# Kernel tuning notes

Hardware: AMD Instinct MI355X
Metric: run time of the kernel (lower is better)

## Reference

```python
import jax, jax.numpy as jnp
import numpy as np

N_POINTS = 300000
N_PAIRS = 100000  # rulebook pairs per kernel offset
K_OFFSETS = 27    # 3x3x3 kernel
C_IN, C_OUT = 32, 64
GROUPS = 8
EPS = 1e-5
NEG_SLOPE = 0.01


def setup_inputs() -> dict:
    key = jax.random.key(0)
    k1, k2, k3, k4 = jax.random.split(key, 4)
    feats = jax.random.normal(k1, (N_POINTS, C_IN), dtype=jnp.float32)
    weight = jax.random.normal(k2, (K_OFFSETS, C_IN, C_OUT), dtype=jnp.float32) * (1.0 / np.sqrt(C_IN * K_OFFSETS))
    gamma = jnp.ones((C_OUT,), dtype=jnp.float32)
    beta = jnp.zeros((C_OUT,), dtype=jnp.float32)
    in_idx = jax.random.randint(k3, (K_OFFSETS, N_PAIRS), 0, N_POINTS, dtype=jnp.int64)
    out_idx = jax.random.randint(k4, (K_OFFSETS, N_PAIRS), 0, N_POINTS, dtype=jnp.int64)
    return {"feats": feats, "weight": weight, "gamma": gamma, "beta": beta,
            "in_idx": in_idx, "out_idx": out_idx}


def reference(feats, weight, gamma, beta, in_idx, out_idx):
    # Sparse 3D conv via rulebook: gather -> per-offset matmul -> scatter-add
    gathered = feats[in_idx]                       # [K, P, C_in]
    y = jnp.einsum('kpi,kio->kpo', gathered, weight)  # [K, P, C_out]
    out = jnp.zeros((feats.shape[0], weight.shape[2]), feats.dtype)
    out = out.at[out_idx.reshape(-1)].add(y.reshape(-1, weight.shape[2]))
    # GroupNorm(8, C_out): stats over all points and channels within each group
    N, C = out.shape
    xg = out.reshape(N, GROUPS, C // GROUPS)
    mean = jnp.mean(xg, axis=(0, 2), keepdims=True)
    var = jnp.var(xg, axis=(0, 2), keepdims=True)
    xn = ((xg - mean) * jax.lax.rsqrt(var + EPS)).reshape(N, C)
    xn = xn * gamma + beta
    # LeakyReLU (default negative_slope = 0.01)
    return jnp.where(xn >= 0, xn, NEG_SLOPE * xn)
```

## Files before the change

kernel.cpp:

```cpp
#include <hip/hip_runtime.h>

#define NPTS   300000
#define NPAIRS 100000
#define KOFF   27
#define NTOT   (KOFF * NPAIRS)
#define CIN    32
#define COUT   64
#define NGROUP 8
#define EPSV   1e-5f
#define SLOPE  0.01f

#define PAIRS_PER_BLOCK 256
#define BLOCKS_PER_K ((NPAIRS + PAIRS_PER_BLOCK - 1) / PAIRS_PER_BLOCK)
#define NB1 293

#define OFS_STATS  0u
#define OFS_CURSOR 4096u
#define OFS_PART   (OFS_CURSOR + 1204224u)
#define OFS_ENT    (OFS_PART + 4096u)
#define OFS_FH16   (OFS_ENT + 10850304u)
#define WS_MAIN    ((size_t)OFS_FH16 + 19200000u)
#define OFS_FB16_FB 4096u
#define WS_BF16_FB ((size_t)OFS_FB16_FB + 19200000u)

typedef _Float16 half2v __attribute__((ext_vector_type(2)));

__device__ inline unsigned pack_h2(float a, float b) {
    union { _Float16 h[2]; unsigned u; } x;
    x.h[0] = (_Float16)a; x.h[1] = (_Float16)b;
    return x.u;
}
__device__ inline half2v as_h2(unsigned u) {
    union { unsigned u; half2v h; } x; x.u = u; return x.h;
}
__device__ inline float dot2_h(unsigned a, unsigned b, float c) {
#if __has_builtin(__builtin_amdgcn_fdot2)
    return __builtin_amdgcn_fdot2(as_h2(a), as_h2(b), c, false);
#else
    half2v ha = as_h2(a), hb = as_h2(b);
    c = fmaf((float)ha.x, (float)hb.x, c);
    return fmaf((float)ha.y, (float)hb.y, c);
#endif
}
__device__ inline unsigned short f2b(float x) {
    unsigned u = __float_as_uint(x);
    u += 0x7FFFu + ((u >> 16) & 1u);
    return (unsigned short)(u >> 16);
}
__device__ inline float b2f_lo(unsigned d) { return __uint_as_float(d << 16); }
__device__ inline float b2f_hi(unsigned d) { return __uint_as_float(d & 0xFFFF0000u); }


__global__ __launch_bounds__(256) void to_f16_kernel(const float2* __restrict__ src,
                                                     unsigned* __restrict__ dst, int n2) {
    int i = blockIdx.x * 256 + threadIdx.x;
    if (i < n2) { float2 v = src[i]; dst[i] = pack_h2(v.x, v.y); }
}

__global__ __launch_bounds__(256) void zero_aux_kernel(int* __restrict__ cursor,
                                                       float* __restrict__ stats) {
    int i = blockIdx.x * 256 + threadIdx.x;
    if (i < NPTS) cursor[i] = 0;
    if (blockIdx.x == 0 && threadIdx.x < 16) stats[threadIdx.x] = 0.f;
}

__global__ __launch_bounds__(256) void hist_kernel(const int* __restrict__ oi,
                                                   int* __restrict__ cursor) {
    int i = blockIdx.x * 256 + threadIdx.x;
    if (i < NTOT) atomicAdd(cursor + oi[i], 1);
}

__global__ __launch_bounds__(256) void reduce_blocks_kernel(const int* __restrict__ cursor,
                                                            int* __restrict__ part) {
    __shared__ int sm[256];
    int tid = threadIdx.x, i0 = blockIdx.x * 1024 + tid * 4;
    int s = 0;
#pragma unroll
    for (int j = 0; j < 4; ++j) if (i0 + j < NPTS) s += cursor[i0 + j];
    sm[tid] = s; __syncthreads();
    for (int off = 128; off; off >>= 1) {
        if (tid < off) sm[tid] += sm[tid + off];
        __syncthreads();
    }
    if (tid == 0) part[blockIdx.x] = sm[0];
}

__global__ __launch_bounds__(512) void scan_partials_kernel(int* __restrict__ part) {
    __shared__ int sm[512];
    int tid = threadIdx.x;
    int v = (tid < NB1) ? part[tid] : 0;
    sm[tid] = v; __syncthreads();
    for (int off = 1; off < 512; off <<= 1) {
        int t = (tid >= off) ? sm[tid - off] : 0;
        __syncthreads();
        sm[tid] += t;
        __syncthreads();
    }
    if (tid < NB1) part[tid] = sm[tid] - v;
}

__global__ __launch_bounds__(256) void scan_apply_kernel(int* __restrict__ cursor,
                                                         const int* __restrict__ part) {
    __shared__ int sm[256];
    int tid = threadIdx.x, i0 = blockIdx.x * 1024 + tid * 4;
    int c0 = 0, c1 = 0, c2 = 0, c3 = 0;
    if (i0 + 0 < NPTS) c0 = cursor[i0 + 0];
    if (i0 + 1 < NPTS) c1 = cursor[i0 + 1];
    if (i0 + 2 < NPTS) c2 = cursor[i0 + 2];
    if (i0 + 3 < NPTS) c3 = cursor[i0 + 3];
    int s = c0 + c1 + c2 + c3;
    sm[tid] = s; __syncthreads();
    for (int off = 1; off < 256; off <<= 1) {
        int t = (tid >= off) ? sm[tid - off] : 0;
        __syncthreads();
        sm[tid] += t;
        __syncthreads();
    }
    int excl = sm[tid] - s + part[blockIdx.x];
    if (i0 + 0 < NPTS) cursor[i0 + 0] = excl;
    if (i0 + 1 < NPTS) cursor[i0 + 1] = excl + c0;
    if (i0 + 2 < NPTS) cursor[i0 + 2] = excl + c0 + c1;
    if (i0 + 3 < NPTS) cursor[i0 + 3] = excl + c0 + c1 + c2;
}

__global__ __launch_bounds__(256) void fill_kernel(const int* __restrict__ oi,
                                                   const int* __restrict__ ii,
                                                   int* __restrict__ cursor,
                                                   unsigned* __restrict__ entries) {
    int i = blockIdx.x * 256 + threadIdx.x;
    if (i < NTOT) {
        int k = i / NPAIRS;
        int slot = atomicAdd(cursor + oi[i], 1);
        entries[slot] = (unsigned)ii[i] | ((unsigned)k << 19);
    }
}

__global__ __launch_bounds__(1024) void conv_csr_kernel(
    const unsigned* __restrict__ fh16, const float* __restrict__ weight,
    const unsigned* __restrict__ entries, const int* __restrict__ ends,
    float* __restrict__ out, float* __restrict__ stats)
{
    __shared__ unsigned lds_w[KOFF * 16 * 64];
    const int tid = threadIdx.x;
    for (int d = tid; d < KOFF * 1024; d += 1024) {
        int k = d >> 10, rem = d & 1023, j = rem >> 6, c = rem & 63;
        const float* wp = weight + k * (CIN * COUT) + (2 * j) * COUT + c;
        lds_w[d] = pack_h2(wp[0], wp[COUT]);
    }
    __syncthreads();

    const int lane = tid & 63;
    const int gw   = blockIdx.x * 16 + (tid >> 6);
    const int chunk = (NPTS + 4095) / 4096;
    int rbeg = gw * chunk;
    int rend = rbeg + chunk; if (rend > NPTS) rend = NPTS;

    float ssum = 0.f, ssq = 0.f;

    if (rbeg < NPTS) {
        int s = (rbeg == 0) ? 0 : ends[rbeg - 1];
        s = __builtin_amdgcn_readfirstlane(s);
        for (int r = rbeg; r < rend; ++r) {
            int e = __builtin_amdgcn_readfirstlane(ends[r]);
            float acc = 0.f;
            if (s < e) {
                unsigned ent = __builtin_amdgcn_readfirstlane(entries[s]);
                unsigned f[16];
                {
                    const unsigned* fr = fh16 + (size_t)(ent & 0x7FFFFu) * 16;
#pragma unroll
                    for (int j = 0; j < 16; ++j) f[j] = fr[j];
                }
                for (int t = s; t < e; ++t) {
                    unsigned nent = (t + 1 < e)
                        ? __builtin_amdgcn_readfirstlane(entries[t + 1]) : ent;
                    unsigned g[16];
                    const unsigned* nr = fh16 + (size_t)(nent & 0x7FFFFu) * 16;
#pragma unroll
                    for (int j = 0; j < 16; ++j) g[j] = nr[j];
                    int kk = ent >> 19;
                    const unsigned* wl = lds_w + (kk << 10) + lane;
#pragma unroll
                    for (int j = 0; j < 16; ++j)
                        acc = dot2_h(f[j], wl[j << 6], acc);
#pragma unroll
                    for (int j = 0; j < 16; ++j) f[j] = g[j];
                    ent = nent;
                }
            }
            out[(size_t)r * COUT + lane] = acc;
            ssum += acc; ssq += acc * acc;
            s = e;
        }
    }
#pragma unroll
    for (int m = 1; m < 8; m <<= 1) {
        ssum += __shfl_xor(ssum, m, 64);
        ssq  += __shfl_xor(ssq,  m, 64);
    }
    if ((lane & 7) == 0) {
        int g = lane >> 3;
        atomicAdd(stats + g,     ssum);
        atomicAdd(stats + 8 + g, ssq);
    }
}

__global__ __launch_bounds__(256) void norm_kernel(float4* __restrict__ out4, int n4,
                                                   const float* __restrict__ stats,
                                                   const float* __restrict__ gamma,
                                                   const float* __restrict__ beta) {
    int i = blockIdx.x * blockDim.x + threadIdx.x;
    if (i >= n4) return;
    int c0 = (i & 15) * 4;
    int g  = c0 >> 3;
    const float cnt = (float)NPTS * (COUT / NGROUP);
    float mean = stats[g] / cnt;
    float var  = stats[8 + g] / cnt - mean * mean;
    float inv  = rsqrtf(var + EPSV);
    float4 v  = out4[i];
    float4 ga = *(const float4*)(gamma + c0);
    float4 be = *(const float4*)(beta  + c0);
    float x;
    x = (v.x - mean) * inv * ga.x + be.x; v.x = x >= 0.f ? x : SLOPE * x;
    x = (v.y - mean) * inv * ga.y + be.y; v.y = x >= 0.f ? x : SLOPE * x;
    x = (v.z - mean) * inv * ga.z + be.z; v.z = x >= 0.f ? x : SLOPE * x;
    x = (v.w - mean) * inv * ga.w + be.w; v.w = x >= 0.f ? x : SLOPE * x;
    out4[i] = v;
}

__global__ __launch_bounds__(256) void zero_kernel(float4* __restrict__ out4, int n4,
                                                   float* __restrict__ stats) {
    int i = blockIdx.x * blockDim.x + threadIdx.x;
    if (i < n4) out4[i] = make_float4(0.f, 0.f, 0.f, 0.f);
    if (blockIdx.x == 0 && threadIdx.x < 16) stats[threadIdx.x] = 0.f;
}

__global__ __launch_bounds__(256) void to_bf16_kernel(const float2* __restrict__ src,
                                                      unsigned* __restrict__ dst, int n2) {
    int i = blockIdx.x * 256 + threadIdx.x;
    if (i < n2) {
        float2 v = src[i];
        dst[i] = (unsigned)f2b(v.x) | ((unsigned)f2b(v.y) << 16);
    }
}

__global__ __launch_bounds__(256) void conv_bf16_kernel(
    const unsigned* __restrict__ fb16, const float* __restrict__ weight,
    const int* __restrict__ in_idx, const int* __restrict__ out_idx,
    float* __restrict__ out)
{
    const int lane = threadIdx.x & 63;
    const int wave = threadIdx.x >> 6;
    const int k     = blockIdx.x / BLOCKS_PER_K;
    const int pair0 = (blockIdx.x % BLOCKS_PER_K) * PAIRS_PER_BLOCK;
    float w[CIN];
    const float* wk = weight + k * (CIN * COUT) + lane;
#pragma unroll
    for (int i = 0; i < CIN; ++i) w[i] = wk[i * COUT];
    const int per_wave = PAIRS_PER_BLOCK / 4;
    int p = pair0 + wave * per_wave;
    int pend = p + per_wave; if (pend > NPAIRS) pend = NPAIRS;
    const int* ii = in_idx  + k * NPAIRS;
    const int* oi = out_idx + k * NPAIRS;
    for (; p < pend; ++p) {
        int rin  = __builtin_amdgcn_readfirstlane(ii[p]);
        int rout = __builtin_amdgcn_readfirstlane(oi[p]);
        const unsigned* fr = fb16 + (size_t)rin * (CIN / 2);
        float acc = 0.f;
#pragma unroll
        for (int j = 0; j < CIN / 2; ++j) {
            unsigned d = fr[j];
            acc = fmaf(b2f_lo(d), w[2 * j],     acc);
            acc = fmaf(b2f_hi(d), w[2 * j + 1], acc);
        }
        atomicAdd(out + (size_t)rout * COUT + lane, acc);
    }
}

__global__ __launch_bounds__(256) void conv_f32_kernel(
    const float* __restrict__ feats, const float* __restrict__ weight,
    const int* __restrict__ in_idx, const int* __restrict__ out_idx,
    float* __restrict__ out)
{
    const int lane = threadIdx.x & 63;
    const int wave = threadIdx.x >> 6;
    const int k     = blockIdx.x / BLOCKS_PER_K;
    const int pair0 = (blockIdx.x % BLOCKS_PER_K) * PAIRS_PER_BLOCK;
    float w[CIN];
    const float* wk = weight + k * (CIN * COUT) + lane;
#pragma unroll
    for (int i = 0; i < CIN; ++i) w[i] = wk[i * COUT];
    const int per_wave = PAIRS_PER_BLOCK / 4;
    int p = pair0 + wave * per_wave;
    int pend = p + per_wave; if (pend > NPAIRS) pend = NPAIRS;
    const int* ii = in_idx  + k * NPAIRS;
    const int* oi = out_idx + k * NPAIRS;
    for (; p < pend; ++p) {
        int rin  = __builtin_amdgcn_readfirstlane(ii[p]);
        int rout = __builtin_amdgcn_readfirstlane(oi[p]);
        const float* frow = feats + (size_t)rin * CIN;
        float acc = 0.f;
#pragma unroll
        for (int i = 0; i < CIN; ++i) acc = fmaf(frow[i], w[i], acc);
        atomicAdd(out + (size_t)rout * COUT + lane, acc);
    }
}

__global__ __launch_bounds__(256) void stats_kernel(const float* __restrict__ out,
                                                    float* __restrict__ stats) {
    const int c = threadIdx.x & 63;
    const int wave_in_grid = blockIdx.x * 4 + (threadIdx.x >> 6);
    const int nwaves = gridDim.x * 4;
    float s = 0.f, ss = 0.f;
    for (int r = wave_in_grid; r < NPTS; r += nwaves) {
        float v = out[(size_t)r * COUT + c];
        s += v; ss += v * v;
    }
#pragma unroll
    for (int m = 1; m < 8; m <<= 1) {
        s  += __shfl_xor(s,  m, 64);
        ss += __shfl_xor(ss, m, 64);
    }
    if ((c & 7) == 0) {
        int g = c >> 3;
        atomicAdd(stats + g,     s);
        atomicAdd(stats + 8 + g, ss);
    }
}

extern "C" void kernel_launch(void* const* d_in, const int* in_sizes, int n_in,
                              void* d_out, int out_size, void* d_ws, size_t ws_size,
                              hipStream_t stream) {
    const float* feats   = (const float*)d_in[0];
    const float* weight  = (const float*)d_in[1];
    const float* gamma   = (const float*)d_in[2];
    const float* beta    = (const float*)d_in[3];
    const int*   in_idx  = (const int*)d_in[4];
    const int*   out_idx = (const int*)d_in[5];
    float* out = (float*)d_out;
    char*  ws  = (char*)d_ws;

    int n4 = out_size / 4;
    int zb = (n4 + 255) / 256;
    int n2 = NPTS * CIN / 2;

    if (ws_size >= WS_MAIN) {
        float*    stats   = (float*)(ws + OFS_STATS);
        int*      cursor  = (int*)(ws + OFS_CURSOR);
        int*      part    = (int*)(ws + OFS_PART);
        unsigned* entries = (unsigned*)(ws + OFS_ENT);
        unsigned* fh16    = (unsigned*)(ws + OFS_FH16);

        to_f16_kernel<<<(n2 + 255) / 256, 256, 0, stream>>>((const float2*)feats, fh16, n2);
        zero_aux_kernel<<<(NPTS + 255) / 256, 256, 0, stream>>>(cursor, (float*)(ws + OFS_STATS));
        hist_kernel<<<(NTOT + 255) / 256, 256, 0, stream>>>(out_idx, cursor);
        reduce_blocks_kernel<<<NB1, 256, 0, stream>>>(cursor, part);
        scan_partials_kernel<<<1, 512, 0, stream>>>(part);
        scan_apply_kernel<<<NB1, 256, 0, stream>>>(cursor, part);
        fill_kernel<<<(NTOT + 255) / 256, 256, 0, stream>>>(out_idx, in_idx, cursor, entries);
        conv_csr_kernel<<<256, 1024, 0, stream>>>(fh16, weight, entries, cursor, out, stats);
        norm_kernel<<<zb, 256, 0, stream>>>((float4*)out, n4, stats, gamma, beta);
    } else if (ws_size >= WS_BF16_FB) {
        float*    stats = (float*)(ws + OFS_STATS);
        unsigned* fb16  = (unsigned*)(ws + OFS_FB16_FB);
        zero_kernel<<<zb, 256, 0, stream>>>((float4*)out, n4, stats);
        to_bf16_kernel<<<(n2 + 255) / 256, 256, 0, stream>>>((const float2*)feats, fb16, n2);
        conv_bf16_kernel<<<KOFF * BLOCKS_PER_K, 256, 0, stream>>>(fb16, weight, in_idx, out_idx, out);
        stats_kernel<<<2048, 256, 0, stream>>>(out, stats);
        norm_kernel<<<zb, 256, 0, stream>>>((float4*)out, n4, stats, gamma, beta);
    } else {
        float* stats = (float*)(ws + OFS_STATS);
        zero_kernel<<<zb, 256, 0, stream>>>((float4*)out, n4, stats);
        conv_f32_kernel<<<KOFF * BLOCKS_PER_K, 256, 0, stream>>>(feats, weight, in_idx, out_idx, out);
        stats_kernel<<<2048, 256, 0, stream>>>(out, stats);
        norm_kernel<<<zb, 256, 0, stream>>>((float4*)out, n4, stats, gamma, beta);
    }
}
```

Measured before the change: 847.1 us.

## Bucket rulebook by 256-row block and offset, accumulate in LDS per block

Replaces the per-output-row CSR with buckets keyed by (256-row block, kernel offset). Each wave then holds a single offset's weights in registers, and each block accumulates its 256 output rows in shared memory with LDS atomics before writing them out and computing the stats. This makes the scan far shorter (about 32K buckets instead of 300K rows) and removes the serial per-row chains and the per-pair LDS weight reads. It also fuses the prep kernels and precomputes the packed weights once. The costs are LDS atomic contention and load imbalance across offsets within a block, since 27 offsets are spread over 16 waves. The bf16 fallback path is also removed.

After: 1.545 ms. +82.4%, slower.

```diff
diff --git a/kernel.cpp b/kernel.cpp
--- a/kernel.cpp
+++ b/kernel.cpp
@@ -10,18 +10,21 @@
 #define EPSV   1e-5f
 #define SLOPE  0.01f
 
+#define RB_SIZE 256
+#define NRB     ((NPTS + RB_SIZE - 1) / RB_SIZE)
+#define NBUK    (NRB * KOFF)
+#define NB2     ((NBUK + 1023) / 1024)
+
 #define PAIRS_PER_BLOCK 256
 #define BLOCKS_PER_K ((NPAIRS + PAIRS_PER_BLOCK - 1) / PAIRS_PER_BLOCK)
-#define NB1 293
 
 #define OFS_STATS  0u
-#define OFS_CURSOR 4096u
-#define OFS_PART   (OFS_CURSOR + 1204224u)
-#define OFS_ENT    (OFS_PART + 4096u)
-#define OFS_FH16   (OFS_ENT + 10850304u)
+#define OFS_PART   4096u
+#define OFS_CURSOR 8192u
+#define OFS_WPK    (OFS_CURSOR + 131072u)
+#define OFS_ENT    (OFS_WPK + 114688u)
+#define OFS_FH16   (OFS_ENT + 10800128u)
 #define WS_MAIN    ((size_t)OFS_FH16 + 19200000u)
-#define OFS_FB16_FB 4096u
-#define WS_BF16_FB ((size_t)OFS_FB16_FB + 19200000u)
 
 typedef _Float16 half2v __attribute__((ext_vector_type(2)));
 
@@ -42,32 +45,32 @@
     return fmaf((float)ha.y, (float)hb.y, c);
 #endif
 }
-__device__ inline unsigned short f2b(float x) {
-    unsigned u = __float_as_uint(x);
-    u += 0x7FFFu + ((u >> 16) & 1u);
-    return (unsigned short)(u >> 16);
-}
-__device__ inline float b2f_lo(unsigned d) { return __uint_as_float(d << 16); }
-__device__ inline float b2f_hi(unsigned d) { return __uint_as_float(d & 0xFFFF0000u); }
-
-
-__global__ __launch_bounds__(256) void to_f16_kernel(const float2* __restrict__ src,
-                                                     unsigned* __restrict__ dst, int n2) {
+
+__global__ __launch_bounds__(256) void prep_kernel(const float2* __restrict__ src, int n2,
+                                                   unsigned* __restrict__ fh16,
+                                                   const float* __restrict__ weight,
+                                                   unsigned* __restrict__ wpk,
+                                                   int* __restrict__ cursor,
+                                                   float* __restrict__ stats) {
     int i = blockIdx.x * 256 + threadIdx.x;
-    if (i < n2) { float2 v = src[i]; dst[i] = pack_h2(v.x, v.y); }
-}
-
-__global__ __launch_bounds__(256) void zero_aux_kernel(int* __restrict__ cursor,
-                                                       float* __restrict__ stats) {
-    int i = blockIdx.x * 256 + threadIdx.x;
-    if (i < NPTS) cursor[i] = 0;
-    if (blockIdx.x == 0 && threadIdx.x < 16) stats[threadIdx.x] = 0.f;
+    if (i < n2) { float2 v = src[i]; fh16[i] = pack_h2(v.x, v.y); }
+    if (i < KOFF * 16 * 64) {
+        int k = i >> 10, rem = i & 1023, j = rem >> 6, c = rem & 63;
+        const float* wp = weight + k * (CIN * COUT) + (2 * j) * COUT + c;
+        wpk[i] = pack_h2(wp[0], wp[COUT]);
+    }
+    if (i < NBUK) cursor[i] = 0;
+    if (i < 16) stats[i] = 0.f;
 }
 
 __global__ __launch_bounds__(256) void hist_kernel(const int* __restrict__ oi,
                                                    int* __restrict__ cursor) {
     int i = blockIdx.x * 256 + threadIdx.x;
-    if (i < NTOT) atomicAdd(cursor + oi[i], 1);
+    if (i < NTOT) {
+        int k = i / NPAIRS;
+        int r = oi[i];
+        atomicAdd(cursor + ((r >> 8) * KOFF + k), 1);
+    }
 }
 
 __global__ __launch_bounds__(256) void reduce_blocks_kernel(const int* __restrict__ cursor,
@@ -76,7 +79,7 @@
     int tid = threadIdx.x, i0 = blockIdx.x * 1024 + tid * 4;
     int s = 0;
 #pragma unroll
-    for (int j = 0; j < 4; ++j) if (i0 + j < NPTS) s += cursor[i0 + j];
+    for (int j = 0; j < 4; ++j) if (i0 + j < NBUK) s += cursor[i0 + j];
     sm[tid] = s; __syncthreads();
     for (int off = 128; off; off >>= 1) {
         if (tid < off) sm[tid] += sm[tid + off];
@@ -85,18 +88,16 @@
     if (tid == 0) part[blockIdx.x] = sm[0];
 }
 
-__global__ __launch_bounds__(512) void scan_partials_kernel(int* __restrict__ part) {
-    __shared__ int sm[512];
+__global__ __launch_bounds__(64) void scan_partials_kernel(int* __restrict__ part) {
     int tid = threadIdx.x;
-    int v = (tid < NB1) ? part[tid] : 0;
-    sm[tid] = v; __syncthreads();
-    for (int off = 1; off < 512; off <<= 1) {
-        int t = (tid >= off) ? sm[tid - off] : 0;
-        __syncthreads();
-        sm[tid] += t;
-        __syncthreads();
-    }
-    if (tid < NB1) part[tid] = sm[tid] - v;
+    int o = (tid < NB2) ? part[tid] : 0;
+    int v = o;
+#pragma unroll
+    for (int off = 1; off < 64; off <<= 1) {
+        int t = __shfl_up(v, off, 64);
+        if (tid >= off) v += t;
+    }
+    if (tid < NB2) part[tid] = v - o;
 }
 
 __global__ __launch_bounds__(256) void scan_apply_kernel(int* __restrict__ cursor,
@@ -104,10 +105,10 @@
     __shared__ int sm[256];
     int tid = threadIdx.x, i0 = blockIdx.x * 1024 + tid * 4;
     int c0 = 0, c1 = 0, c2 = 0, c3 = 0;
-    if (i0 + 0 < NPTS) c0 = cursor[i0 + 0];
-    if (i0 + 1 < NPTS) c1 = cursor[i0 + 1];
-    if (i0 + 2 < NPTS) c2 = cursor[i0 + 2];
-    if (i0 + 3 < NPTS) c3 = cursor[i0 + 3];
+    if (i0 + 0 < NBUK) c0 = cursor[i0 + 0];
+    if (i0 + 1 < NBUK) c1 = cursor[i0 + 1];
+    if (i0 + 2 < NBUK) c2 = cursor[i0 + 2];
+    if (i0 + 3 < NBUK) c3 = cursor[i0 + 3];
     int s = c0 + c1 + c2 + c3;
     sm[tid] = s; __syncthreads();
     for (int off = 1; off < 256; off <<= 1) {
@@ -117,10 +118,10 @@
         __syncthreads();
     }
     int excl = sm[tid] - s + part[blockIdx.x];
-    if (i0 + 0 < NPTS) cursor[i0 + 0] = excl;
-    if (i0 + 1 < NPTS) cursor[i0 + 1] = excl + c0;
-    if (i0 + 2 < NPTS) cursor[i0 + 2] = excl + c0 + c1;
-    if (i0 + 3 < NPTS) cursor[i0 + 3] = excl + c0 + c1 + c2;
+    if (i0 + 0 < NBUK) cursor[i0 + 0] = excl;
+    if (i0 + 1 < NBUK) cursor[i0 + 1] = excl + c0;
+    if (i0 + 2 < NBUK) cursor[i0 + 2] = excl + c0 + c1;
+    if (i0 + 3 < NBUK) cursor[i0 + 3] = excl + c0 + c1 + c2;
 }
 
 __global__ __launch_bounds__(256) void fill_kernel(const int* __restrict__ oi,
@@ -130,67 +131,84 @@
     int i = blockIdx.x * 256 + threadIdx.x;
     if (i < NTOT) {
         int k = i / NPAIRS;
-        int slot = atomicAdd(cursor + oi[i], 1);
-        entries[slot] = (unsigned)ii[i] | ((unsigned)k << 19);
-    }
-}
-
-__global__ __launch_bounds__(1024) void conv_csr_kernel(
-    const unsigned* __restrict__ fh16, const float* __restrict__ weight,
-    const unsigned* __restrict__ entries, const int* __restrict__ ends,
+        int r = oi[i];
+        int slot = atomicAdd(cursor + ((r >> 8) * KOFF + k), 1);
+        entries[slot] = (unsigned)ii[i] | ((unsigned)(r & 255) << 19);
+    }
+}
+
+__global__ __launch_bounds__(1024) void conv_bucket_kernel(
+    const unsigned* __restrict__ fh16, const unsigned* __restrict__ wpk,
+    const unsigned* __restrict__ entries, const int* __restrict__ cursor,
     float* __restrict__ out, float* __restrict__ stats)
 {
-    __shared__ unsigned lds_w[KOFF * 16 * 64];
-    const int tid = threadIdx.x;
-    for (int d = tid; d < KOFF * 1024; d += 1024) {
-        int k = d >> 10, rem = d & 1023, j = rem >> 6, c = rem & 63;
-        const float* wp = weight + k * (CIN * COUT) + (2 * j) * COUT + c;
-        lds_w[d] = pack_h2(wp[0], wp[COUT]);
-    }
+    __shared__ float4 smv[RB_SIZE * COUT / 4];
+    float* sm = (float*)smv;
+    const int tid  = threadIdx.x;
+    const int lane = tid & 63;
+    const int wv   = tid >> 6;
+
+#pragma unroll
+    for (int j = 0; j < 4; ++j)
+        smv[tid + j * 1024] = make_float4(0.f, 0.f, 0.f, 0.f);
     __syncthreads();
 
-    const int lane = tid & 63;
-    const int gw   = blockIdx.x * 16 + (tid >> 6);
-    const int chunk = (NPTS + 4095) / 4096;
-    int rbeg = gw * chunk;
-    int rend = rbeg + chunk; if (rend > NPTS) rend = NPTS;
+    const int rb = blockIdx.x;
+
+    for (int kk = wv; kk < KOFF; kk += 16) {
+        int key = rb * KOFF + kk;
+        int s = (key == 0) ? 0 : cursor[key - 1];
+        int e = cursor[key];
+        s = __builtin_amdgcn_readfirstlane(s);
+        e = __builtin_amdgcn_readfirstlane(e);
+        if (s >= e) continue;
+
+        unsigned w[16];
+        const unsigned* wp = wpk + (kk << 10) + lane;
+#pragma unroll
+        for (int j = 0; j < 16; ++j) w[j] = wp[j << 6];
+
+        for (int base = s; base < e; base += 64) {
+            int nv = e - base; if (nv > 64) nv = 64;
+            unsigned entv = 0;
+            if (base + lane < e) entv = entries[base + lane];
+#pragma unroll 2
+            for (int t = 0; t < nv; ++t) {
+                unsigned ent = __shfl(entv, t, 64);
+                const uint4* fr = (const uint4*)(fh16 + (size_t)(ent & 0x7FFFFu) * 16);
+                uint4 fa = fr[0], fb = fr[1], fc = fr[2], fd = fr[3];
+                float acc = 0.f;
+                acc = dot2_h(fa.x, w[0],  acc);
+                acc = dot2_h(fa.y, w[1],  acc);
+                acc = dot2_h(fa.z, w[2],  acc);
+                acc = dot2_h(fa.w, w[3],  acc);
+                acc = dot2_h(fb.x, w[4],  acc);
+                acc = dot2_h(fb.y, w[5],  acc);
+                acc = dot2_h(fb.z, w[6],  acc);
+                acc = dot2_h(fb.w, w[7],  acc);
+                acc = dot2_h(fc.x, w[8],  acc);
+                acc = dot2_h(fc.y, w[9],  acc);
+                acc = dot2_h(fc.z, w[10], acc);
+                acc = dot2_h(fc.w, w[11], acc);
+                acc = dot2_h(fd.x, w[12], acc);
+                acc = dot2_h(fd.y, w[13], acc);
+                acc = dot2_h(fd.z, w[14], acc);
+                acc = dot2_h(fd.w, w[15], acc);
+                int lr = (int)(ent >> 19);
+                atomicAdd(&sm[(lr << 6) + lane], acc);
+            }
+        }
+    }
+    __syncthreads();
 
     float ssum = 0.f, ssq = 0.f;
-
-    if (rbeg < NPTS) {
-        int s = (rbeg == 0) ? 0 : ends[rbeg - 1];
-        s = __builtin_amdgcn_readfirstlane(s);
-        for (int r = rbeg; r < rend; ++r) {
-            int e = __builtin_amdgcn_readfirstlane(ends[r]);
-            float acc = 0.f;
-            if (s < e) {
-                unsigned ent = __builtin_amdgcn_readfirstlane(entries[s]);
-                unsigned f[16];
-                {
-                    const unsigned* fr = fh16 + (size_t)(ent & 0x7FFFFu) * 16;
-#pragma unroll
-                    for (int j = 0; j < 16; ++j) f[j] = fr[j];
-                }
-                for (int t = s; t < e; ++t) {
-                    unsigned nent = (t + 1 < e)
-                        ? __builtin_amdgcn_readfirstlane(entries[t + 1]) : ent;
-                    unsigned g[16];
-                    const unsigned* nr = fh16 + (size_t)(nent & 0x7FFFFu) * 16;
-#pragma unroll
-                    for (int j = 0; j < 16; ++j) g[j] = nr[j];
-                    int kk = ent >> 19;
-                    const unsigned* wl = lds_w + (kk << 10) + lane;
-#pragma unroll
-                    for (int j = 0; j < 16; ++j)
-                        acc = dot2_h(f[j], wl[j << 6], acc);
-#pragma unroll
-                    for (int j = 0; j < 16; ++j) f[j] = g[j];
-                    ent = nent;
-                }
-            }
-            out[(size_t)r * COUT + lane] = acc;
-            ssum += acc; ssq += acc * acc;
-            s = e;
+    int r0 = rb << 8;
+    for (int lr = wv; lr < RB_SIZE; lr += 16) {
+        int gr = r0 + lr;
+        if (gr < NPTS) {
+            float v = sm[(lr << 6) + lane];
+            out[(size_t)gr * COUT + lane] = v;
+            ssum += v; ssq += v * v;
         }
     }
 #pragma unroll
@@ -199,9 +217,8 @@
         ssq  += __shfl_xor(ssq,  m, 64);
     }
     if ((lane & 7) == 0) {
-        int g = lane >> 3;
-        atomicAdd(stats + g,     ssum);
-        atomicAdd(stats + 8 + g, ssq);
+        atomicAdd(stats + (lane >> 3),     ssum);
+        atomicAdd(stats + 8 + (lane >> 3), ssq);
     }
 }
 
@@ -235,48 +252,6 @@
     if (blockIdx.x == 0 && threadIdx.x < 16) stats[threadIdx.x] = 0.f;
 }
 
-__global__ __launch_bounds__(256) void to_bf16_kernel(const float2* __restrict__ src,
-                                                      unsigned* __restrict__ dst, int n2) {
-    int i = blockIdx.x * 256 + threadIdx.x;
-    if (i < n2) {
-        float2 v = src[i];
-        dst[i] = (unsigned)f2b(v.x) | ((unsigned)f2b(v.y) << 16);
-    }
-}
-
-__global__ __launch_bounds__(256) void conv_bf16_kernel(
-    const unsigned* __restrict__ fb16, const float* __restrict__ weight,
-    const int* __restrict__ in_idx, const int* __restrict__ out_idx,
-    float* __restrict__ out)
-{
-    const int lane = threadIdx.x & 63;
-    const int wave = threadIdx.x >> 6;
-    const int k     = blockIdx.x / BLOCKS_PER_K;
-    const int pair0 = (blockIdx.x % BLOCKS_PER_K) * PAIRS_PER_BLOCK;
-    float w[CIN];
-    const float* wk = weight + k * (CIN * COUT) + lane;
-#pragma unroll
-    for (int i = 0; i < CIN; ++i) w[i] = wk[i * COUT];
-    const int per_wave = PAIRS_PER_BLOCK / 4;
-    int p = pair0 + wave * per_wave;
-    int pend = p + per_wave; if (pend > NPAIRS) pend = NPAIRS;
-    const int* ii = in_idx  + k * NPAIRS;
-    const int* oi = out_idx + k * NPAIRS;
-    for (; p < pend; ++p) {
-        int rin  = __builtin_amdgcn_readfirstlane(ii[p]);
-        int rout = __builtin_amdgcn_readfirstlane(oi[p]);
-        const unsigned* fr = fb16 + (size_t)rin * (CIN / 2);
-        float acc = 0.f;
-#pragma unroll
-        for (int j = 0; j < CIN / 2; ++j) {
-            unsigned d = fr[j];
-            acc = fmaf(b2f_lo(d), w[2 * j],     acc);
-            acc = fmaf(b2f_hi(d), w[2 * j + 1], acc);
-        }
-        atomicAdd(out + (size_t)rout * COUT + lane, acc);
-    }
-}
-
 __global__ __launch_bounds__(256) void conv_f32_kernel(
     const float* __restrict__ feats, const float* __restrict__ weight,
     const int* __restrict__ in_idx, const int* __restrict__ out_idx,
@@ -322,9 +297,8 @@
         ss += __shfl_xor(ss, m, 64);
     }
     if ((c & 7) == 0) {
-        int g = c >> 3;
-        atomicAdd(stats + g,     s);
-        atomicAdd(stats + 8 + g, ss);
+        atomicAdd(stats + (c >> 3),     s);
+        atomicAdd(stats + 8 + (c >> 3), ss);
     }
 }
 
@@ -342,31 +316,24 @@
 
     int n4 = out_size / 4;
     int zb = (n4 + 255) / 256;
-    int n2 = NPTS * CIN / 2;
 
     if (ws_size >= WS_MAIN) {
         float*    stats   = (float*)(ws + OFS_STATS);
+        int*      part    = (int*)(ws + OFS_PART);
         int*      cursor  = (int*)(ws + OFS_CURSOR);
-        int*      part    = (int*)(ws + OFS_PART);
+        unsigned* wpk     = (unsigned*)(ws + OFS_WPK);
         unsigned* entries = (unsigned*)(ws + OFS_ENT);
         unsigned* fh16    = (unsigned*)(ws + OFS_FH16);
-
-        to_f16_kernel<<<(n2 + 255) / 256, 256, 0, stream>>>((const float2*)feats, fh16, n2);
-        zero_aux_kernel<<<(NPTS + 255) / 256, 256, 0, stream>>>(cursor, (float*)(ws + OFS_STATS));
+        int n2 = NPTS * CIN / 2;
+
+        prep_kernel<<<(n2 + 255) / 256, 256, 0, stream>>>((const float2*)feats, n2,
+                                                          fh16, weight, wpk, cursor, stats);
         hist_kernel<<<(NTOT + 255) / 256, 256, 0, stream>>>(out_idx, cursor);
-        reduce_blocks_kernel<<<NB1, 256, 0, stream>>>(cursor, part);
-        scan_partials_kernel<<<1, 512, 0, stream>>>(part);
-        scan_apply_kernel<<<NB1, 256, 0, stream>>>(cursor, part);
+        reduce_blocks_kernel<<<NB2, 256, 0, stream>>>(cursor, part);
+        scan_partials_kernel<<<1, 64, 0, stream>>>(part);
+        scan_apply_kernel<<<NB2, 256, 0, stream>>>(cursor, part);
         fill_kernel<<<(NTOT + 255) / 256, 256, 0, stream>>>(out_idx, in_idx, cursor, entries);
-        conv_csr_kernel<<<256, 1024, 0, stream>>>(fh16, weight, entries, cursor, out, stats);
-        norm_kernel<<<zb, 256, 0, stream>>>((float4*)out, n4, stats, gamma, beta);
-    } else if (ws_size >= WS_BF16_FB) {
-        float*    stats = (float*)(ws + OFS_STATS);
-        unsigned* fb16  = (unsigned*)(ws + OFS_FB16_FB);
-        zero_kernel<<<zb, 256, 0, stream>>>((float4*)out, n4, stats);
-        to_bf16_kernel<<<(n2 + 255) / 256, 256, 0, stream>>>((const float2*)feats, fb16, n2);
-        conv_bf16_kernel<<<KOFF * BLOCKS_PER_K, 256, 0, stream>>>(fb16, weight, in_idx, out_idx, out);
-        stats_kernel<<<2048, 256, 0, stream>>>(out, stats);
+        conv_bucket_kernel<<<NRB, 1024, 0, stream>>>(fh16, wpk, entries, cursor, out, stats);
         norm_kernel<<<zb, 256, 0, stream>>>((float4*)out, n4, stats, gamma, beta);
     } else {
         float* stats = (float*)(ws + OFS_STATS);
```
